# Optimization experiments

Measured on AMD Instinct MI355X. Metric: run time of the kernel, lower is better.

The kernel has to match this reference:

```python
import jax, jax.numpy as jnp
import numpy as np

NUM_HEADS = 4


def _conv1x1(W, b, x):
    # nn.Conv1d(d_model, d_model, kernel_size=1): pointwise channel mix
    return jnp.einsum('oi,bin->bon', W, x) + b[None, :, None]


def _rot3d_rel_position(desc0, pos, lrf):
    # desc0: [b, d, h, n_pts], pos: [b, n, m, 3], lrf: [b, n, 3, 3] (n == n_pts == m)
    b, d, h, npts = desc0.shape
    m = pos.shape[2]
    # rotate-half: pairs (x0, x1) -> (-x1, x0)
    dh = desc0.reshape(b, d // 2, 2, h, npts)
    desc = jnp.concatenate([-dh[:, :, 1:2], dh[:, :, 0:1]], axis=2).reshape(b, d, h, npts)
    # rotate relative positions into each point's local reference frame
    # torch: einsum('bnxy,bnmy->bnmx', lrf.transpose(2,3), pos) == einsum('bnyx,bnmy->bnmx', lrf, pos)
    posl = jnp.einsum('bnyx,bnmy->bnmx', lrf, pos)
    px, py, pz = posl[..., 0], posl[..., 1], posl[..., 2]
    alpha = jnp.arctan(py / px)
    alpha = jnp.where(px < 0, alpha + np.pi, alpha)
    phi = jnp.arctan(pz / jnp.sqrt(px * px + py * py))
    alpha = jnp.where(jnp.isnan(alpha), 0.0, alpha)
    phi = jnp.where(jnp.isnan(phi), 0.0, phi)
    # F.interpolate(nearest, [m,4]) on [b,n,m,2] duplicates the last axis: [a,a,p,p]
    rot = jnp.stack([alpha, alpha, phi, phi], axis=-1)      # [b,n,m,4]
    rot = jnp.tile(rot, (1, 1, 1, d // 4))                  # [b,n,m,d] (head-independent)
    # 5D rotated value tensor (faithful to original math; head axis broadcast)
    return (jnp.einsum('bdhn,bnmd->bdhnm', desc0, jnp.cos(rot))
            + jnp.einsum('bdhn,bnmd->bdhnm', desc, jnp.sin(rot)))


def setup_inputs() -> dict:
    key = jax.random.key(0)
    ks = jax.random.split(key, 13)
    b, d_model, n, m = 4, 256, 256, 256
    s = 1.0 / np.sqrt(d_model)
    inp = {
        'x': jax.random.normal(ks[0], (b, d_model, n), dtype=jnp.float32),
        'source': jax.random.normal(ks[1], (b, d_model, m), dtype=jnp.float32),
        'x_pos': jax.random.normal(ks[2], (b, n, 3), dtype=jnp.float32),
        'src_pos': jax.random.normal(ks[3], (b, m, 3), dtype=jnp.float32),
        'lrf': jax.random.normal(ks[4], (b, n, 3, 3), dtype=jnp.float32),
        'Wq': jax.random.normal(ks[5], (d_model, d_model), dtype=jnp.float32) * s,
        'bq': jax.random.normal(ks[6], (d_model,), dtype=jnp.float32) * 0.02,
        'Wk': jax.random.normal(ks[7], (d_model, d_model), dtype=jnp.float32) * s,
        'bk': jax.random.normal(ks[8], (d_model,), dtype=jnp.float32) * 0.02,
        'Wv': jax.random.normal(ks[9], (d_model, d_model), dtype=jnp.float32) * s,
        'bv': jax.random.normal(ks[10], (d_model,), dtype=jnp.float32) * 0.02,
        'Wm': jax.random.normal(ks[11], (d_model, d_model), dtype=jnp.float32) * s,
        'bm': jax.random.normal(ks[12], (d_model,), dtype=jnp.float32) * 0.02,
        'k': 32,
    }
    return inp


def reference(x, source, x_pos, src_pos, lrf, Wq, bq, Wk, bk, Wv, bv, Wm, bm, k):
    b, d_model, n = x.shape
    m = source.shape[2]
    h = NUM_HEADS
    dim = d_model // h
    q = _conv1x1(Wq, bq, x).reshape(b, dim, h, n)
    key_ = _conv1x1(Wk, bk, source).reshape(b, dim, h, m)
    val = _conv1x1(Wv, bv, source).reshape(b, dim, h, m)
    # 'self' branch: 3D rotary relative-position encoding of values
    rel = x_pos[:, :, None, :] - src_pos[:, None, :, :]  # [b,n,m,3]
    value5 = _rot3d_rel_position(val, rel, lrf)          # [b,dim,h,n,m]
    # dynamic (top-k sparsified) attention
    scores = jnp.einsum('bdhn,bdhm->bhnm', q, key_) / np.float32(dim) ** 0.5
    vals, idx = jax.lax.top_k(scores, k)                 # over key axis m
    probs = jax.nn.softmax(vals, axis=-1)
    bi = jnp.arange(b)[:, None, None, None]
    hi = jnp.arange(h)[None, :, None, None]
    ni = jnp.arange(n)[None, None, :, None]
    sparse = jnp.zeros_like(scores).at[bi, hi, ni, idx].set(probs)
    # note the deliberate m<->n swap on value5 as in the original einsum
    out = jnp.einsum('bhnm,bdhmn->bdhn', sparse, value5)
    return _conv1x1(Wm, bm, out.reshape(b, d_model, n))
```

## Files before the change

### kernel.cpp

```cpp
#include <hip/hip_runtime.h>
#include <math.h>

#define DM 256
#define NP 256
#define NH 4
#define DH 64

typedef unsigned long long u64;
typedef unsigned int u32;

__global__ __launch_bounds__(256) void qkv_part_kernel(
    const float* __restrict__ x, const float* __restrict__ src,
    const float* __restrict__ Wq, const float* __restrict__ Wk,
    const float* __restrict__ Wv,
    float* __restrict__ Ppart)
{
  const int tile = blockIdx.x;
  const int mat  = blockIdx.y;
  const int bz   = blockIdx.z;
  const int b  = bz >> 1;
  const int ks = bz & 1;
  const int tc = (tile >> 2) * 64;
  const int tp = (tile & 3) * 64;
  const float* W = (mat == 0) ? Wq : (mat == 1) ? Wk : Wv;
  const float* X = ((mat == 0) ? x : src) + (size_t)b * DM * NP;
  float* P = Ppart + ((size_t)((ks * 3 + mat) * 4 + b)) * 65536;

  __shared__ float Ws[2][32][64];
  __shared__ float Xs[2][32][64];
  const int tid = threadIdx.x;
  const int ty = tid >> 4, tx = tid & 15;
  const int c0 = tid >> 3;
  const int k4 = tid & 7;
  const int pX = tid & 15;
  const int kX = tid >> 4;
  const int kbase = ks * 128;

  float4 wA, wB, xA, xB;
  #define LOADQKV(K0)                                                          \
    wA = *(const float4*)&W[(size_t)(tc + c0)      * DM + (K0) + k4 * 4];      \
    wB = *(const float4*)&W[(size_t)(tc + c0 + 32) * DM + (K0) + k4 * 4];      \
    xA = *(const float4*)&X[(size_t)((K0) + kX)      * NP + tp + pX * 4];      \
    xB = *(const float4*)&X[(size_t)((K0) + kX + 16) * NP + tp + pX * 4];

  #define STOREQKV(BUF)                                                        \
    Ws[BUF][k4*4+0][c0] = wA.x; Ws[BUF][k4*4+1][c0] = wA.y;                    \
    Ws[BUF][k4*4+2][c0] = wA.z; Ws[BUF][k4*4+3][c0] = wA.w;                    \
    Ws[BUF][k4*4+0][c0+32] = wB.x; Ws[BUF][k4*4+1][c0+32] = wB.y;              \
    Ws[BUF][k4*4+2][c0+32] = wB.z; Ws[BUF][k4*4+3][c0+32] = wB.w;              \
    *(float4*)&Xs[BUF][kX][pX*4]      = xA;                                    \
    *(float4*)&Xs[BUF][kX+16][pX*4]   = xB;

  LOADQKV(kbase);
  STOREQKV(0);
  __syncthreads();

  float acc[4][4];
  #pragma unroll
  for (int i = 0; i < 4; ++i)
    #pragma unroll
    for (int j = 0; j < 4; ++j) acc[i][j] = 0.f;

  for (int ch = 0; ch < 4; ++ch) {
    const int cur = ch & 1;
    if (ch < 3) { LOADQKV(kbase + (ch + 1) * 32); }
    #pragma unroll
    for (int kk = 0; kk < 32; ++kk) {
      float4 a = *(const float4*)&Ws[cur][kk][ty * 4];
      float4 xv = *(const float4*)&Xs[cur][kk][tx * 4];
      float av[4] = {a.x, a.y, a.z, a.w};
      float xvv[4] = {xv.x, xv.y, xv.z, xv.w};
      #pragma unroll
      for (int i = 0; i < 4; ++i)
        #pragma unroll
        for (int j = 0; j < 4; ++j) acc[i][j] += av[i] * xvv[j];
    }
    if (ch < 3) {
      STOREQKV(cur ^ 1);
      __syncthreads();
    }
  }

  #pragma unroll
  for (int i = 0; i < 4; ++i) {
    float4 o4;
    o4.x = acc[i][0]; o4.y = acc[i][1]; o4.z = acc[i][2]; o4.w = acc[i][3];
    *(float4*)&P[(size_t)(tc + ty * 4 + i) * NP + tp + tx * 4] = o4;
  }
  #undef LOADQKV
  #undef STOREQKV
}

__global__ __launch_bounds__(256) void score_gemm_kernel(
    const float* __restrict__ Ppart,
    const float* __restrict__ bq, const float* __restrict__ bk,
    const float* __restrict__ bv,
    float* __restrict__ scores, float* __restrict__ Vt)
{
  const int tile = blockIdx.x;
  const int bh   = blockIdx.y;
  const int tn = (tile >> 2) * 64;
  const int tm = (tile & 3) * 64;
  const int b = bh >> 2, h = bh & 3;

  const float* PQ0 = Ppart + ((size_t)( 0 + b)) * 65536;
  const float* PQ1 = Ppart + ((size_t)(12 + b)) * 65536;
  const float* PK0 = Ppart + ((size_t)( 4 + b)) * 65536;
  const float* PK1 = Ppart + ((size_t)(16 + b)) * 65536;
  const float* PV0 = Ppart + ((size_t)( 8 + b)) * 65536;
  const float* PV1 = Ppart + ((size_t)(20 + b)) * 65536;

  __shared__ float Qs[64][68];
  __shared__ float Ks[64][68];
  __shared__ float Vs[16][68];
  const int tid = threadIdx.x;

  #pragma unroll
  for (int pass = 0; pass < 4; ++pass) {
    const int u  = tid + pass * 256;
    const int pg = u & 15;
    const int d  = u >> 4;
    const int c  = d * 4 + h;
    const float bqv = bq[c], bkv = bk[c];
    const float4 q0 = *(const float4*)&PQ0[(size_t)c * NP + tn + pg * 4];
    const float4 q1 = *(const float4*)&PQ1[(size_t)c * NP + tn + pg * 4];
    const float4 k0 = *(const float4*)&PK0[(size_t)c * NP + tm + pg * 4];
    const float4 k1 = *(const float4*)&PK1[(size_t)c * NP + tm + pg * 4];
    Qs[d][pg*4+0] = q0.x + q1.x + bqv;
    Qs[d][pg*4+1] = q0.y + q1.y + bqv;
    Qs[d][pg*4+2] = q0.z + q1.z + bqv;
    Qs[d][pg*4+3] = q0.w + q1.w + bqv;
    Ks[d][pg*4+0] = k0.x + k1.x + bkv;
    Ks[d][pg*4+1] = k0.y + k1.y + bkv;
    Ks[d][pg*4+2] = k0.z + k1.z + bkv;
    Ks[d][pg*4+3] = k0.w + k1.w + bkv;
  }
  __syncthreads();

  const int ty = tid >> 4, tx = tid & 15;
  float acc[4][4];
  #pragma unroll
  for (int i = 0; i < 4; ++i)
    #pragma unroll
    for (int j = 0; j < 4; ++j) acc[i][j] = 0.f;

  #pragma unroll 4
  for (int d = 0; d < DH; ++d) {
    const float4 a  = *(const float4*)&Qs[d][ty * 4];
    const float4 bvv4 = *(const float4*)&Ks[d][tx * 4];
    const float av[4]  = {a.x, a.y, a.z, a.w};
    const float bvv[4] = {bvv4.x, bvv4.y, bvv4.z, bvv4.w};
    #pragma unroll
    for (int i = 0; i < 4; ++i)
      #pragma unroll
      for (int j = 0; j < 4; ++j) acc[i][j] += av[i] * bvv[j];
  }

  float* srow = scores + ((size_t)bh * NP + tn) * NP + tm;
  #pragma unroll
  for (int i = 0; i < 4; ++i) {
    float4 o4;
    o4.x = acc[i][0] * 0.125f; o4.y = acc[i][1] * 0.125f;
    o4.z = acc[i][2] * 0.125f; o4.w = acc[i][3] * 0.125f;
    *(float4*)&srow[(size_t)(ty * 4 + i) * NP + tx * 4] = o4;
  }

  {
    const int dV = tid >> 2;
    const int mg = tid & 3;
    const int cV = dV * 4 + h;
    const float bvb = bv[cV];
    const float4 v0 = *(const float4*)&PV0[(size_t)cV * NP + tile * 16 + mg * 4];
    const float4 v1 = *(const float4*)&PV1[(size_t)cV * NP + tile * 16 + mg * 4];
    Vs[mg*4+0][dV] = v0.x + v1.x + bvb;
    Vs[mg*4+1][dV] = v0.y + v1.y + bvb;
    Vs[mg*4+2][dV] = v0.z + v1.z + bvb;
    Vs[mg*4+3][dV] = v0.w + v1.w + bvb;
  }
  __syncthreads();
  {
    const int mrow = tid >> 4;
    const int dg   = tid & 15;
    const float4 o = *(const float4*)&Vs[mrow][dg * 4];
    *(float4*)&Vt[((size_t)bh * NP + tile * 16 + mrow) * DH + dg * 4] = o;
  }
}

__global__ __launch_bounds__(256) void attn_topk_kernel(
    const float* __restrict__ scores, const float* __restrict__ Vt,
    const float* __restrict__ x_pos, const float* __restrict__ src_pos,
    const float* __restrict__ lrf,
    const int* __restrict__ kptr,
    float* __restrict__ O)
{
  const int tid  = threadIdx.x;
  const int wid  = tid >> 6;
  const int lane = tid & 63;
  const int bidx = blockIdx.x;
  const int rb   = (bidx & 7) * 128 + (bidx >> 3);
  const int row  = rb * 4 + wid;
  const int n    = row & (NP - 1);
  const int bh   = row >> 8;
  const int b    = bh >> 2;
  const int h    = bh & 3;

  int kk = *kptr;
  if (kk > 64) kk = 64;
  if (kk < 1) kk = 1;

  __shared__ float  eslot[4][64];
  __shared__ int    msel[4][64];
  __shared__ float4 ang[4][64];
  __shared__ float  otile[4][64];

  const float4 s4 = *(const float4*)&scores[(size_t)row * NP + lane * 4];
  float s[4] = { s4.x, s4.y, s4.z, s4.w };
  u32 u[4], lowv[4];
  #pragma unroll
  for (int r = 0; r < 4; ++r) {
    u32 bb = __float_as_uint(s[r]);
    u[r] = (bb & 0x80000000u) ? ~bb : (bb | 0x80000000u);
    lowv[r] = (u32)(255 - (lane * 4 + r));
  }

  u32 T = 0u;
  #pragma unroll
  for (int bit = 31; bit >= 0; --bit) {
    const u32 cand = T | (1u << bit);
    int c = 0;
    #pragma unroll
    for (int r = 0; r < 4; ++r) c += __popcll(__ballot(u[r] >= cand));
    if (c >= kk) T = cand;
  }
  int c_gt = 0;
  #pragma unroll
  for (int r = 0; r < 4; ++r) c_gt += __popcll(__ballot(u[r] > T));

  u32 Lo = 0u;
  #pragma unroll
  for (int bit = 7; bit >= 0; --bit) {
    const u32 cand = Lo | (1u << bit);
    int c = c_gt;
    #pragma unroll
    for (int r = 0; r < 4; ++r)
      c += __popcll(__ballot((u[r] == T) && (lowv[r] >= cand)));
    if (c >= kk) Lo = cand;
  }

  const float sT = __uint_as_float((T & 0x80000000u) ? (T & 0x7fffffffu) : ~T);
  bool sel[4]; float e[4]; u64 selm[4];
  #pragma unroll
  for (int r = 0; r < 4; ++r) {
    sel[r] = (u[r] > T) || ((u[r] == T) && (lowv[r] >= Lo));
    e[r] = sel[r] ? expf(s[r] - sT) : 0.f;
    selm[r] = __ballot(sel[r]);
  }
  float z = e[0] + e[1] + e[2] + e[3];
  #pragma unroll
  for (int off = 32; off; off >>= 1) z += __shfl_xor(z, off);

  const u64 lt = (1ull << lane) - 1ull;
  int base = 0;
  #pragma unroll
  for (int r = 0; r < 4; ++r) {
    if (sel[r]) {
      const int slot = base + __popcll(selm[r] & lt);
      eslot[wid][slot] = e[r];
      msel[wid][slot]  = lane * 4 + r;
    }
    base += __popcll(selm[r]);
  }

  if (lane < kk) {
    const float ej = eslot[wid][lane];
    const int   mj = msel[wid][lane];
    const float p = ej / z;
    const float* xp = x_pos   + ((size_t)b * NP + mj) * 3;
    const float* sp = src_pos + ((size_t)b * NP + n) * 3;
    const float* L  = lrf     + ((size_t)b * NP + mj) * 9;
    const float r0 = xp[0] - sp[0], r1 = xp[1] - sp[1], r2v = xp[2] - sp[2];
    const float px = L[0]*r0 + L[3]*r1 + L[6]*r2v;
    const float py = L[1]*r0 + L[4]*r1 + L[7]*r2v;
    const float pz = L[2]*r0 + L[5]*r1 + L[8]*r2v;
    const float r2 = px*px + py*py;
    const float inv2 = (r2 > 0.f) ? rsqrtf(r2) : 0.f;
    const float ca = (r2 > 0.f) ? px * inv2 : 1.f;
    const float sa = py * inv2;
    const float r2d = r2 * inv2;
    const float r3 = r2 + pz * pz;
    const float inv3 = (r3 > 0.f) ? rsqrtf(r3) : 0.f;
    const float cph = (r3 > 0.f) ? r2d * inv3 : 1.f;
    const float sph = pz * inv3;
    ang[wid][lane] = make_float4(p * ca, p * sa, p * cph, p * sph);
  }

  const float* vbase = Vt + (size_t)bh * NP * DH;
  const bool useA = ((lane & 3) < 2);
  const bool odd  = (lane & 1);
  const int  ev   = lane & ~1;
  float acc = 0.f;

  #define ACCSTEP(V2, A4) {                                                   \
    const float vm  = odd ? (V2).y :  (V2).x;                                 \
    const float dsc = odd ? (V2).x : -(V2).y;                                 \
    acc += vm  * (useA ? (A4).x : (A4).z)                                     \
         + dsc * (useA ? (A4).y : (A4).w); }

  int j = 0;
  float2 v0, v1, v2, v3;
  if (kk >= 4) {
    const int a0 = msel[wid][0], a1 = msel[wid][1];
    const int a2 = msel[wid][2], a3 = msel[wid][3];
    v0 = *(const float2*)(vbase + (size_t)a0 * DH + ev);
    v1 = *(const float2*)(vbase + (size_t)a1 * DH + ev);
    v2 = *(const float2*)(vbase + (size_t)a2 * DH + ev);
    v3 = *(const float2*)(vbase + (size_t)a3 * DH + ev);
  }
  for (; j + 8 <= kk; j += 4) {
    const int n0 = msel[wid][j+4], n1 = msel[wid][j+5];
    const int n2 = msel[wid][j+6], n3 = msel[wid][j+7];
    const float2 w0 = *(const float2*)(vbase + (size_t)n0 * DH + ev);
    const float2 w1 = *(const float2*)(vbase + (size_t)n1 * DH + ev);
    const float2 w2 = *(const float2*)(vbase + (size_t)n2 * DH + ev);
    const float2 w3 = *(const float2*)(vbase + (size_t)n3 * DH + ev);
    const float4 A0 = ang[wid][j],   A1 = ang[wid][j+1];
    const float4 A2 = ang[wid][j+2], A3 = ang[wid][j+3];
    ACCSTEP(v0, A0); ACCSTEP(v1, A1); ACCSTEP(v2, A2); ACCSTEP(v3, A3);
    v0 = w0; v1 = w1; v2 = w2; v3 = w3;
  }
  if (j + 4 <= kk) {
    const float4 A0 = ang[wid][j],   A1 = ang[wid][j+1];
    const float4 A2 = ang[wid][j+2], A3 = ang[wid][j+3];
    ACCSTEP(v0, A0); ACCSTEP(v1, A1); ACCSTEP(v2, A2); ACCSTEP(v3, A3);
    j += 4;
  }
  for (; j < kk; ++j) {
    const int m = msel[wid][j];
    const float2 vv = *(const float2*)(vbase + (size_t)m * DH + ev);
    const float4 A  = ang[wid][j];
    ACCSTEP(vv, A);
  }
  #undef ACCSTEP

  otile[wid][lane] = acc;
  __syncthreads();
  if (wid == 0) {
    float4 o4;
    o4.x = otile[0][lane]; o4.y = otile[1][lane];
    o4.z = otile[2][lane]; o4.w = otile[3][lane];
    const int c = (lane << 2) | h;
    const int n0 = (rb * 4) & (NP - 1);
    *(float4*)&O[((size_t)b * DM + c) * NP + n0] = o4;
  }
}

__global__ __launch_bounds__(256) void final_part_kernel(
    const float* __restrict__ O, const float* __restrict__ Wm,
    float* __restrict__ Pf)
{
  const int tile = blockIdx.x;
  const int ks   = blockIdx.y;
  const int b    = blockIdx.z;
  const int tc = (tile >> 2) * 64;
  const int tp = (tile & 3) * 64;
  const float* X = O + (size_t)b * DM * NP;
  float* P = Pf + (size_t)ks * (DM * NP * 4) + (size_t)b * DM * NP;

  __shared__ float Ws[2][32][64];
  __shared__ float Xs[2][32][64];
  const int tid = threadIdx.x;
  const int ty = tid >> 4, tx = tid & 15;
  const int c0 = tid >> 3;
  const int k4 = tid & 7;
  const int pX = tid & 15;
  const int kX = tid >> 4;
  const int kbase = ks * 64;

  float4 wA, wB, xA, xB;
  #define LOADF(K0)                                                            \
    wA = *(const float4*)&Wm[(size_t)(tc + c0)      * DM + (K0) + k4 * 4];     \
    wB = *(const float4*)&Wm[(size_t)(tc + c0 + 32) * DM + (K0) + k4 * 4];     \
    xA = *(const float4*)&X[(size_t)((K0) + kX)      * NP + tp + pX * 4];      \
    xB = *(const float4*)&X[(size_t)((K0) + kX + 16) * NP + tp + pX * 4];

  #define STOREF(BUF)                                                          \
    Ws[BUF][k4*4+0][c0] = wA.x; Ws[BUF][k4*4+1][c0] = wA.y;                    \
    Ws[BUF][k4*4+2][c0] = wA.z; Ws[BUF][k4*4+3][c0] = wA.w;                    \
    Ws[BUF][k4*4+0][c0+32] = wB.x; Ws[BUF][k4*4+1][c0+32] = wB.y;              \
    Ws[BUF][k4*4+2][c0+32] = wB.z; Ws[BUF][k4*4+3][c0+32] = wB.w;              \
    *(float4*)&Xs[BUF][kX][pX*4]      = xA;                                    \
    *(float4*)&Xs[BUF][kX+16][pX*4]   = xB;

  LOADF(kbase);
  STOREF(0);
  __syncthreads();

  float acc[4][4];
  #pragma unroll
  for (int i = 0; i < 4; ++i)
    #pragma unroll
    for (int j = 0; j < 4; ++j) acc[i][j] = 0.f;

  for (int ch = 0; ch < 2; ++ch) {
    const int cur = ch & 1;
    if (ch < 1) { LOADF(kbase + 32); }
    #pragma unroll
    for (int kk = 0; kk < 32; ++kk) {
      float4 a = *(const float4*)&Ws[cur][kk][ty * 4];
      float4 xv = *(const float4*)&Xs[cur][kk][tx * 4];
      float av[4] = {a.x, a.y, a.z, a.w};
      float xvv[4] = {xv.x, xv.y, xv.z, xv.w};
      #pragma unroll
      for (int i = 0; i < 4; ++i)
        #pragma unroll
        for (int j = 0; j < 4; ++j) acc[i][j] += av[i] * xvv[j];
    }
    if (ch < 1) {
      STOREF(cur ^ 1);
      __syncthreads();
    }
  }

  #pragma unroll
  for (int i = 0; i < 4; ++i) {
    float4 o4;
    o4.x = acc[i][0]; o4.y = acc[i][1]; o4.z = acc[i][2]; o4.w = acc[i][3];
    *(float4*)&P[(size_t)(tc + ty * 4 + i) * NP + tp + tx * 4] = o4;
  }
  #undef LOADF
  #undef STOREF
}

__global__ __launch_bounds__(256) void final_merge_kernel(
    const float* __restrict__ Pf, const float* __restrict__ bm,
    float* __restrict__ out)
{
  const int u = blockIdx.x * 256 + threadIdx.x;
  const int c = (u >> 6) & 255;
  const float bb = bm[c];
  const size_t stride = (size_t)DM * NP * 4 / 4;
  const float4* P4 = (const float4*)Pf;
  float4 a = P4[u];
  float4 b2 = P4[u + stride];
  float4 c2 = P4[u + 2 * stride];
  float4 d2 = P4[u + 3 * stride];
  float4 o;
  o.x = a.x + b2.x + c2.x + d2.x + bb;
  o.y = a.y + b2.y + c2.y + d2.y + bb;
  o.z = a.z + b2.z + c2.z + d2.z + bb;
  o.w = a.w + b2.w + c2.w + d2.w + bb;
  ((float4*)out)[u] = o;
}

extern "C" void kernel_launch(void* const* d_in, const int* in_sizes, int n_in,
                              void* d_out, int out_size, void* d_ws, size_t ws_size,
                              hipStream_t stream)
{
  const float* x       = (const float*)d_in[0];
  const float* source  = (const float*)d_in[1];
  const float* x_pos   = (const float*)d_in[2];
  const float* src_pos = (const float*)d_in[3];
  const float* lrf     = (const float*)d_in[4];
  const float* Wq = (const float*)d_in[5];
  const float* bq = (const float*)d_in[6];
  const float* Wk = (const float*)d_in[7];
  const float* bk = (const float*)d_in[8];
  const float* Wv = (const float*)d_in[9];
  const float* bv = (const float*)d_in[10];
  const float* Wm = (const float*)d_in[11];
  const float* bm = (const float*)d_in[12];
  const int* kptr = (const int*)d_in[13];
  float* out = (float*)d_out;

  float* ws = (float*)d_ws;
  float* Ppart  = ws;
  float* scores = Ppart + 1572864;
  float* Vt     = scores + 1048576;
  float* O      = Vt + 262144;
  float* Pf     = O + 262144;

  qkv_part_kernel<<<dim3(16, 3, 8), 256, 0, stream>>>(
      x, source, Wq, Wk, Wv, Ppart);
  score_gemm_kernel<<<dim3(16, 16), 256, 0, stream>>>(
      Ppart, bq, bk, bv, scores, Vt);
  attn_topk_kernel<<<dim3(1024), 256, 0, stream>>>(
      scores, Vt, x_pos, src_pos, lrf, kptr, O);
  final_part_kernel<<<dim3(16, 4, 4), 256, 0, stream>>>(
      O, Wm, Pf);
  final_merge_kernel<<<dim3(256), 256, 0, stream>>>(
      Pf, bm, out);
}
```

Measured before the change: 43.57 us.

## Read GEMM activation operand directly from global memory and widen gather loop

In the QKV and final projection GEMMs, the activation tile is no longer staged in shared memory. Each thread reads its float4 directly from global memory, relying on cache reuse across the 16 threads that share a column slice, and an extra barrier is added before each weight-buffer store. The top-k gather loop now loads eight selected indices with int4 reads from 16-byte aligned shared memory and issues eight value loads per iteration, replacing the software-pipelined four-wide version. This trades shared-memory traffic and LDS footprint for more global/L1 load latency inside the inner FMA loop.

```diff
diff --git a/kernel.cpp b/kernel.cpp
--- a/kernel.cpp
+++ b/kernel.cpp
@@ -27,32 +27,26 @@
   float* P = Ppart + ((size_t)((ks * 3 + mat) * 4 + b)) * 65536;
 
   __shared__ float Ws[2][32][64];
-  __shared__ float Xs[2][32][64];
   const int tid = threadIdx.x;
   const int ty = tid >> 4, tx = tid & 15;
   const int c0 = tid >> 3;
   const int k4 = tid & 7;
-  const int pX = tid & 15;
-  const int kX = tid >> 4;
   const int kbase = ks * 128;
 
-  float4 wA, wB, xA, xB;
-  #define LOADQKV(K0)                                                          \
+  const float* Xp = X + (size_t)kbase * NP + tp + tx * 4;
+
+  float4 wA, wB;
+  #define LOADW(K0)                                                            \
     wA = *(const float4*)&W[(size_t)(tc + c0)      * DM + (K0) + k4 * 4];      \
-    wB = *(const float4*)&W[(size_t)(tc + c0 + 32) * DM + (K0) + k4 * 4];      \
-    xA = *(const float4*)&X[(size_t)((K0) + kX)      * NP + tp + pX * 4];      \
-    xB = *(const float4*)&X[(size_t)((K0) + kX + 16) * NP + tp + pX * 4];
-
-  #define STOREQKV(BUF)                                                        \
+    wB = *(const float4*)&W[(size_t)(tc + c0 + 32) * DM + (K0) + k4 * 4];
+  #define STOREW(BUF)                                                          \
     Ws[BUF][k4*4+0][c0] = wA.x; Ws[BUF][k4*4+1][c0] = wA.y;                    \
     Ws[BUF][k4*4+2][c0] = wA.z; Ws[BUF][k4*4+3][c0] = wA.w;                    \
     Ws[BUF][k4*4+0][c0+32] = wB.x; Ws[BUF][k4*4+1][c0+32] = wB.y;              \
-    Ws[BUF][k4*4+2][c0+32] = wB.z; Ws[BUF][k4*4+3][c0+32] = wB.w;              \
-    *(float4*)&Xs[BUF][kX][pX*4]      = xA;                                    \
-    *(float4*)&Xs[BUF][kX+16][pX*4]   = xB;
-
-  LOADQKV(kbase);
-  STOREQKV(0);
+    Ws[BUF][k4*4+2][c0+32] = wB.z; Ws[BUF][k4*4+3][c0+32] = wB.w;
+
+  LOADW(kbase);
+  STOREW(0);
   __syncthreads();
 
   float acc[4][4];
@@ -63,20 +57,21 @@
 
   for (int ch = 0; ch < 4; ++ch) {
     const int cur = ch & 1;
-    if (ch < 3) { LOADQKV(kbase + (ch + 1) * 32); }
-    #pragma unroll
+    if (ch < 3) { LOADW(kbase + (ch + 1) * 32); }
+    #pragma unroll 8
     for (int kk = 0; kk < 32; ++kk) {
-      float4 a = *(const float4*)&Ws[cur][kk][ty * 4];
-      float4 xv = *(const float4*)&Xs[cur][kk][tx * 4];
-      float av[4] = {a.x, a.y, a.z, a.w};
-      float xvv[4] = {xv.x, xv.y, xv.z, xv.w};
+      const float4 a  = *(const float4*)&Ws[cur][kk][ty * 4];
+      const float4 xv = *(const float4*)&Xp[(size_t)(ch * 32 + kk) * NP];
+      const float av[4]  = {a.x, a.y, a.z, a.w};
+      const float xvv[4] = {xv.x, xv.y, xv.z, xv.w};
       #pragma unroll
       for (int i = 0; i < 4; ++i)
         #pragma unroll
         for (int j = 0; j < 4; ++j) acc[i][j] += av[i] * xvv[j];
     }
     if (ch < 3) {
-      STOREQKV(cur ^ 1);
+      __syncthreads();
+      STOREW(cur ^ 1);
       __syncthreads();
     }
   }
@@ -87,8 +82,8 @@
     o4.x = acc[i][0]; o4.y = acc[i][1]; o4.z = acc[i][2]; o4.w = acc[i][3];
     *(float4*)&P[(size_t)(tc + ty * 4 + i) * NP + tp + tx * 4] = o4;
   }
-  #undef LOADQKV
-  #undef STOREQKV
+  #undef LOADW
+  #undef STOREW
 }
 
 __global__ __launch_bounds__(256) void score_gemm_kernel(
@@ -209,7 +204,7 @@
   if (kk < 1) kk = 1;
 
   __shared__ float  eslot[4][64];
-  __shared__ int    msel[4][64];
+  __shared__ alignas(16) int msel[4][64];
   __shared__ float4 ang[4][64];
   __shared__ float  otile[4][64];
 
@@ -307,32 +302,25 @@
          + dsc * (useA ? (A4).y : (A4).w); }
 
   int j = 0;
-  float2 v0, v1, v2, v3;
-  if (kk >= 4) {
-    const int a0 = msel[wid][0], a1 = msel[wid][1];
-    const int a2 = msel[wid][2], a3 = msel[wid][3];
-    v0 = *(const float2*)(vbase + (size_t)a0 * DH + ev);
-    v1 = *(const float2*)(vbase + (size_t)a1 * DH + ev);
-    v2 = *(const float2*)(vbase + (size_t)a2 * DH + ev);
-    v3 = *(const float2*)(vbase + (size_t)a3 * DH + ev);
-  }
-  for (; j + 8 <= kk; j += 4) {
-    const int n0 = msel[wid][j+4], n1 = msel[wid][j+5];
-    const int n2 = msel[wid][j+6], n3 = msel[wid][j+7];
-    const float2 w0 = *(const float2*)(vbase + (size_t)n0 * DH + ev);
-    const float2 w1 = *(const float2*)(vbase + (size_t)n1 * DH + ev);
-    const float2 w2 = *(const float2*)(vbase + (size_t)n2 * DH + ev);
-    const float2 w3 = *(const float2*)(vbase + (size_t)n3 * DH + ev);
-    const float4 A0 = ang[wid][j],   A1 = ang[wid][j+1];
-    const float4 A2 = ang[wid][j+2], A3 = ang[wid][j+3];
-    ACCSTEP(v0, A0); ACCSTEP(v1, A1); ACCSTEP(v2, A2); ACCSTEP(v3, A3);
-    v0 = w0; v1 = w1; v2 = w2; v3 = w3;
-  }
-  if (j + 4 <= kk) {
-    const float4 A0 = ang[wid][j],   A1 = ang[wid][j+1];
-    const float4 A2 = ang[wid][j+2], A3 = ang[wid][j+3];
-    ACCSTEP(v0, A0); ACCSTEP(v1, A1); ACCSTEP(v2, A2); ACCSTEP(v3, A3);
-    j += 4;
+  for (; j + 8 <= kk; j += 8) {
+    const int4 mA = *(const int4*)&msel[wid][j];
+    const int4 mB = *(const int4*)&msel[wid][j + 4];
+    const float2 v0 = *(const float2*)(vbase + (size_t)mA.x * DH + ev);
+    const float2 v1 = *(const float2*)(vbase + (size_t)mA.y * DH + ev);
+    const float2 v2 = *(const float2*)(vbase + (size_t)mA.z * DH + ev);
+    const float2 v3 = *(const float2*)(vbase + (size_t)mA.w * DH + ev);
+    const float2 v4 = *(const float2*)(vbase + (size_t)mB.x * DH + ev);
+    const float2 v5 = *(const float2*)(vbase + (size_t)mB.y * DH + ev);
+    const float2 v6 = *(const float2*)(vbase + (size_t)mB.z * DH + ev);
+    const float2 v7 = *(const float2*)(vbase + (size_t)mB.w * DH + ev);
+    const float4 A0 = ang[wid][j+0]; ACCSTEP(v0, A0);
+    const float4 A1 = ang[wid][j+1]; ACCSTEP(v1, A1);
+    const float4 A2 = ang[wid][j+2]; ACCSTEP(v2, A2);
+    const float4 A3 = ang[wid][j+3]; ACCSTEP(v3, A3);
+    const float4 A4 = ang[wid][j+4]; ACCSTEP(v4, A4);
+    const float4 A5 = ang[wid][j+5]; ACCSTEP(v5, A5);
+    const float4 A6 = ang[wid][j+6]; ACCSTEP(v6, A6);
+    const float4 A7 = ang[wid][j+7]; ACCSTEP(v7, A7);
   }
   for (; j < kk; ++j) {
     const int m = msel[wid][j];
@@ -367,32 +355,26 @@
   float* P = Pf + (size_t)ks * (DM * NP * 4) + (size_t)b * DM * NP;
 
   __shared__ float Ws[2][32][64];
-  __shared__ float Xs[2][32][64];
   const int tid = threadIdx.x;
   const int ty = tid >> 4, tx = tid & 15;
   const int c0 = tid >> 3;
   const int k4 = tid & 7;
-  const int pX = tid & 15;
-  const int kX = tid >> 4;
   const int kbase = ks * 64;
 
-  float4 wA, wB, xA, xB;
-  #define LOADF(K0)                                                            \
+  const float* Xp = X + (size_t)kbase * NP + tp + tx * 4;
+
+  float4 wA, wB;
+  #define LOADW(K0)                                                            \
     wA = *(const float4*)&Wm[(size_t)(tc + c0)      * DM + (K0) + k4 * 4];     \
-    wB = *(const float4*)&Wm[(size_t)(tc + c0 + 32) * DM + (K0) + k4 * 4];     \
-    xA = *(const float4*)&X[(size_t)((K0) + kX)      * NP + tp + pX * 4];      \
-    xB = *(const float4*)&X[(size_t)((K0) + kX + 16) * NP + tp + pX * 4];
-
-  #define STOREF(BUF)                                                          \
+    wB = *(const float4*)&Wm[(size_t)(tc + c0 + 32) * DM + (K0) + k4 * 4];
+  #define STOREW(BUF)                                                          \
     Ws[BUF][k4*4+0][c0] = wA.x; Ws[BUF][k4*4+1][c0] = wA.y;                    \
     Ws[BUF][k4*4+2][c0] = wA.z; Ws[BUF][k4*4+3][c0] = wA.w;                    \
     Ws[BUF][k4*4+0][c0+32] = wB.x; Ws[BUF][k4*4+1][c0+32] = wB.y;              \
-    Ws[BUF][k4*4+2][c0+32] = wB.z; Ws[BUF][k4*4+3][c0+32] = wB.w;              \
-    *(float4*)&Xs[BUF][kX][pX*4]      = xA;                                    \
-    *(float4*)&Xs[BUF][kX+16][pX*4]   = xB;
-
-  LOADF(kbase);
-  STOREF(0);
+    Ws[BUF][k4*4+2][c0+32] = wB.z; Ws[BUF][k4*4+3][c0+32] = wB.w;
+
+  LOADW(kbase);
+  STOREW(0);
   __syncthreads();
 
   float acc[4][4];
@@ -403,20 +385,21 @@
 
   for (int ch = 0; ch < 2; ++ch) {
     const int cur = ch & 1;
-    if (ch < 1) { LOADF(kbase + 32); }
-    #pragma unroll
+    if (ch < 1) { LOADW(kbase + 32); }
+    #pragma unroll 8
     for (int kk = 0; kk < 32; ++kk) {
-      float4 a = *(const float4*)&Ws[cur][kk][ty * 4];
-      float4 xv = *(const float4*)&Xs[cur][kk][tx * 4];
-      float av[4] = {a.x, a.y, a.z, a.w};
-      float xvv[4] = {xv.x, xv.y, xv.z, xv.w};
+      const float4 a  = *(const float4*)&Ws[cur][kk][ty * 4];
+      const float4 xv = *(const float4*)&Xp[(size_t)(ch * 32 + kk) * NP];
+      const float av[4]  = {a.x, a.y, a.z, a.w};
+      const float xvv[4] = {xv.x, xv.y, xv.z, xv.w};
       #pragma unroll
       for (int i = 0; i < 4; ++i)
         #pragma unroll
         for (int j = 0; j < 4; ++j) acc[i][j] += av[i] * xvv[j];
     }
     if (ch < 1) {
-      STOREF(cur ^ 1);
+      __syncthreads();
+      STOREW(cur ^ 1);
       __syncthreads();
     }
   }
@@ -427,8 +410,8 @@
     o4.x = acc[i][0]; o4.y = acc[i][1]; o4.z = acc[i][2]; o4.w = acc[i][3];
     *(float4*)&P[(size_t)(tc + ty * 4 + i) * NP + tp + tx * 4] = o4;
   }
-  #undef LOADF
-  #undef STOREF
+  #undef LOADW
+  #undef STOREW
 }
 
 __global__ __launch_bounds__(256) void final_merge_kernel(
```

After: 46.73 us. +7.2%, slower.
